# Kernel optimization log

Measured on AMD Instinct MI355X. Metric: run time of the kernel, lower is better.

## Reference

```python
import jax, jax.numpy as jnp
import numpy as np

B, R, A, S, SR = 128, 1024, 512, 196, 64


def _linear(x, w, b):
    return x @ w.T + b


def _lstm_cell(x, h, c, wih, whh, bih, bhh):
    # torch.nn.LSTMCell gate order: i, f, g, o
    g = x @ wih.T + bih + h @ whh.T + bhh
    i, f, gg, o = jnp.split(g, 4, axis=-1)
    c2 = jax.nn.sigmoid(f) * c + jax.nn.sigmoid(i) * jnp.tanh(gg)
    h2 = jax.nn.sigmoid(o) * jnp.tanh(c2)
    return h2, c2


def _attention(h, att_feats, p_att, mask, h2att_w, h2att_b, aw, ab):
    att_h = _linear(h, h2att_w, h2att_b)[:, None, :]            # [B,1,A]
    dot = jnp.tanh(p_att + att_h)                               # [B,S,A]
    e = jnp.einsum('bsa,a->bs', dot, aw[0]) + ab[0]             # alpha_net
    w = jax.nn.softmax(e, axis=1)
    w = w * mask
    w = w / jnp.sum(w, axis=1, keepdims=True)
    return jnp.einsum('bs,bsd->bd', w, att_feats)


def setup_inputs() -> dict:
    key = jax.random.key(0)
    ks = iter(jax.random.split(key, 80))
    def rn(shape, scale=1.0):
        return jax.random.normal(next(ks), shape, dtype=jnp.float32) * scale
    w = 0.02  # weight init scale
    inp = {
        'xt': rn((B, R)), 'state_h': rn((2, B, R)), 'state_c': rn((2, B, R)),
        'fc_feats': rn((B, R)),
        'att_feats': rn((B, S, R)), 'obj_feats': rn((B, S, R)),
        'attr_feats': rn((B, S, R)), 'rela_feats': rn((B, SR, R)),
        'p_obj_feats': rn((B, S, A)), 'p_attr_feats': rn((B, S, A)),
        'p_rela_feats': rn((B, SR, A)),
        'att_masks': jnp.ones((B, S), jnp.float32),
        'rela_masks': jnp.ones((B, SR), jnp.float32),
        'att_wih': rn((4*R, 3*R), w), 'att_whh': rn((4*R, R), w),
        'att_bih': rn((4*R,), w), 'att_bhh': rn((4*R,), w),
        'lang_wih': rn((4*R, 4*R), w), 'lang_whh': rn((4*R, R), w),
        'lang_bih': rn((4*R,), w), 'lang_bhh': rn((4*R,), w),
        'xt2_w': rn((R, R), w), 'xt2_b': rn((R,), w),
        'h_att2_w': rn((R, R), w), 'h_att2_b': rn((R,), w),
        'r_i2h_w': rn((R, 4*R), w), 'r_i2h_b': rn((R,), w),
        'r_h2h_w': rn((R, R), w), 'r_h2h_b': rn((R,), w),
        'huu_w': rn((R, 3*R), w), 'huu_b': rn((R,), w),
        'obj_h2att_w': rn((A, R), w), 'obj_h2att_b': rn((A,), w),
        'obj_alpha_w': rn((1, A), w), 'obj_alpha_b': rn((1,), w),
        'attr_h2att_w': rn((A, R), w), 'attr_h2att_b': rn((A,), w),
        'attr_alpha_w': rn((1, A), w), 'attr_alpha_b': rn((1,), w),
        'rela_h2att_w': rn((A, R), w), 'rela_h2att_b': rn((A,), w),
        'rela_alpha_w': rn((1, A), w), 'rela_alpha_b': rn((1,), w),
        'fr_lin_w': rn((R, R), w), 'fr_lin_b': rn((R,), w),
        'fr_emb_w': rn((R, R), w), 'fr_emb_b': rn((R,), w),
        'ho_lin_w': rn((R, R), w), 'ho_lin_b': rn((R,), w),
        'ho_emb_w': rn((R, R), w), 'ho_emb_b': rn((R,), w),
        'ada_alpha_w': rn((1, R), w), 'ada_alpha_b': rn((1,), w),
        'cfe_w': rn((R, A), w), 'cfe_b': rn((R,), w),
    }
    return inp


def reference(xt, state_h, state_c, fc_feats, att_feats, obj_feats, attr_feats,
              rela_feats, p_obj_feats, p_attr_feats, p_rela_feats, att_masks,
              rela_masks, att_wih, att_whh, att_bih, att_bhh, lang_wih,
              lang_whh, lang_bih, lang_bhh, xt2_w, xt2_b, h_att2_w, h_att2_b,
              r_i2h_w, r_i2h_b, r_h2h_w, r_h2h_b, huu_w, huu_b, obj_h2att_w,
              obj_h2att_b, obj_alpha_w, obj_alpha_b, attr_h2att_w,
              attr_h2att_b, attr_alpha_w, attr_alpha_b, rela_h2att_w,
              rela_h2att_b, rela_alpha_w, rela_alpha_b, fr_lin_w, fr_lin_b,
              fr_emb_w, fr_emb_b, ho_lin_w, ho_lin_b, ho_emb_w, ho_emb_b,
              ada_alpha_w, ada_alpha_b, cfe_w, cfe_b):
    # eval mode: all dropouts are identity
    prev_h = state_h[1]
    att_in = jnp.concatenate([prev_h, fc_feats, xt], axis=1)            # [B,3R]
    h_att_raw, c_att = _lstm_cell(att_in, state_h[0], state_c[0],
                                  att_wih, att_whh, att_bih, att_bhh)
    h_att = _linear(xt, xt2_w, xt2_b) + _linear(h_att_raw, h_att2_w, h_att2_b)
    att_obj = _attention(h_att, obj_feats, p_obj_feats, att_masks,
                         obj_h2att_w, obj_h2att_b, obj_alpha_w, obj_alpha_b)
    att_attr = _attention(h_att, attr_feats, p_attr_feats, att_masks,
                          attr_h2att_w, attr_h2att_b, attr_alpha_w, attr_alpha_b)
    att_rela = _attention(h_att, rela_feats, p_rela_feats, rela_masks,
                          rela_h2att_w, rela_h2att_b, rela_alpha_w, rela_alpha_b)
    lang_in = jnp.concatenate([h_att, att_obj, att_attr, att_rela], axis=1)  # [B,4R]
    h_lang, c_lang = _lstm_cell(lang_in, state_h[1], state_c[1],
                                lang_wih, lang_whh, lang_bih, lang_bhh)
    tanh_mt = jnp.tanh(c_lang)
    n5 = _linear(lang_in, r_i2h_w, r_i2h_b) + _linear(state_h[1], r_h2h_w, r_h2h_b)
    st = jax.nn.sigmoid(n5) * tanh_mt                                    # [B,R]
    # AdaAtt_attention(h_lang, st, att_feats, p_obj_feats)
    cfe = _linear(p_obj_feats, cfe_w, cfe_b)                             # [B,S,R]
    fake_region = jax.nn.relu(_linear(st, fr_lin_w, fr_lin_b))           # [B,R]
    fr_embed = _linear(fake_region, fr_emb_w, fr_emb_b)
    ho = jnp.tanh(_linear(h_lang, ho_lin_w, ho_lin_b))
    ho_embed = _linear(ho, ho_emb_w, ho_emb_b)
    img_all = jnp.concatenate([fake_region[:, None, :], att_feats], axis=1)    # [B,S+1,R]
    img_all_embed = jnp.concatenate([fr_embed[:, None, :], cfe], axis=1)
    hA = jnp.tanh(img_all_embed + ho_embed[:, None, :])
    e = jnp.einsum('bsr,r->bs', hA, ada_alpha_w[0]) + ada_alpha_b[0]
    PI = jax.nn.softmax(e, axis=1)                                       # [B,S+1]
    visAtt = jnp.einsum('bs,bsd->bd', PI, img_all)
    beta = PI[:, -1:]
    c_t_hat = beta * fake_region + (1.0 - beta) * visAtt
    output = _linear(jnp.concatenate([h_att, h_lang, c_t_hat], axis=1), huu_w, huu_b)
    new_h = jnp.stack([h_att, h_lang])
    new_c = jnp.stack([c_att, c_lang])
    return output, new_h, new_c
```

## Files before the change

kernel.cpp:

```cpp
#include <hip/hip_runtime.h>
#include <cstddef>

#define B 128
#define R 1024

typedef __attribute__((ext_vector_type(8))) short short8;
typedef __attribute__((ext_vector_type(4))) float f32x4;

__device__ __forceinline__ float sigf(float x) { return 1.0f / (1.0f + __expf(-x)); }

__device__ __forceinline__ short f2bf(float f) {
    unsigned int u = __float_as_uint(f);
    u += 0x7fff + ((u >> 16) & 1);
    return (short)(u >> 16);
}

__device__ __forceinline__ float bf2f(short s) {
    unsigned int u = ((unsigned int)(unsigned short)s) << 16;
    return __uint_as_float(u);
}

__device__ __forceinline__ short8 cvt8(float4 u, float4 v) {
    short8 r;
    r[0] = f2bf(u.x); r[1] = f2bf(u.y); r[2] = f2bf(u.z); r[3] = f2bf(u.w);
    r[4] = f2bf(v.x); r[5] = f2bf(v.y); r[6] = f2bf(v.z); r[7] = f2bf(v.w);
    return r;
}

__device__ __forceinline__ void gll16(const void* g, void* l) {
    __builtin_amdgcn_global_load_lds(
        (const __attribute__((address_space(1))) unsigned int*)g,
        (__attribute__((address_space(3))) unsigned int*)l, 16, 0, 0);
}

struct GJob {
    const float* A1; const float* A2; const float* A3;
    const float* W1; const float* W2; const float* W3;
    float* C;
    int lda1, lda2, lda3;
    int ldw1, ldw2, ldw3;
    int K1, K12, Ktot;
    int ldc, Kchunk, nb;
};

__global__ __launch_bounds__(256) void gemm_sk_kernel(GJob j0, GJob j1, GJob j2, int njobs)
{
    GJob j = j0;
    int nbx = blockIdx.x;
    if (njobs > 1 && nbx >= j.nb) { nbx -= j.nb; j = j1; }
    if (njobs > 2 && nbx >= j.nb) { nbx -= j.nb; j = j2; }

    const int bn   = nbx * 64;
    const int kbeg = blockIdx.y * j.Kchunk;
    const int kend = kbeg + j.Kchunk;

    __shared__ short sA[128 * 40];
    __shared__ short sB[64 * 40];
    const int tid  = threadIdx.x;
    const int rA   = tid >> 1;
    const int kha  = (tid & 1) << 4;
    const int rB   = tid >> 2;
    const int khb  = (tid & 3) << 3;
    const int lane = tid & 63;
    const int wid  = tid >> 6;
    const int wm   = wid * 32;
    const int fr_  = lane & 15;
    const int kof  = (lane >> 4) * 8;

    f32x4 acc[2][4];
#pragma unroll
    for (int m = 0; m < 2; ++m)
#pragma unroll
        for (int n = 0; n < 4; ++n)
            acc[m][n] = (f32x4)0.0f;

    for (int k0 = kbeg; k0 < kend; k0 += 32) {
        int kgA = k0 + kha;
        const float* pa;
        if (kgA < j.K1)       pa = j.A1 + (size_t)rA * j.lda1 + kgA;
        else if (kgA < j.K12) pa = j.A2 + (size_t)rA * j.lda2 + (kgA - j.K1);
        else                  pa = j.A3 + (size_t)rA * j.lda3 + (kgA - j.K12);
        int kgB = k0 + khb;
        const float* pw;
        if (kgB < j.K1)       pw = j.W1 + (size_t)(bn + rB) * j.ldw1 + kgB;
        else if (kgB < j.K12) pw = j.W2 + (size_t)(bn + rB) * j.ldw2 + (kgB - j.K1);
        else                  pw = j.W3 + (size_t)(bn + rB) * j.ldw3 + (kgB - j.K12);

        float4 a0 = ((const float4*)pa)[0];
        float4 a1 = ((const float4*)pa)[1];
        float4 a2 = ((const float4*)pa)[2];
        float4 a3 = ((const float4*)pa)[3];
        float4 w0 = ((const float4*)pw)[0];
        float4 w1 = ((const float4*)pw)[1];
        __syncthreads();
        *(short8*)&sA[rA * 40 + kha]     = cvt8(a0, a1);
        *(short8*)&sA[rA * 40 + kha + 8] = cvt8(a2, a3);
        *(short8*)&sB[rB * 40 + khb]     = cvt8(w0, w1);
        __syncthreads();
        short8 af[2], bf[4];
#pragma unroll
        for (int m = 0; m < 2; ++m)
            af[m] = *(const short8*)&sA[(wm + m * 16 + fr_) * 40 + kof];
#pragma unroll
        for (int n = 0; n < 4; ++n)
            bf[n] = *(const short8*)&sB[(n * 16 + fr_) * 40 + kof];
#pragma unroll
        for (int m = 0; m < 2; ++m)
#pragma unroll
            for (int n = 0; n < 4; ++n)
                acc[m][n] = __builtin_amdgcn_mfma_f32_16x16x32_bf16(af[m], bf[n], acc[m][n], 0, 0, 0);
    }

#pragma unroll
    for (int m = 0; m < 2; ++m) {
        int row0 = wm + m * 16 + ((lane >> 4) << 2);
#pragma unroll
        for (int n = 0; n < 4; ++n) {
            int col = bn + n * 16 + fr_;
#pragma unroll
            for (int rg = 0; rg < 4; ++rg)
                atomicAdd(&j.C[(size_t)(row0 + rg) * j.ldc + col], acc[m][n][rg]);
        }
    }
}

__global__ __launch_bounds__(256) void prologue_kernel(
    float* __restrict__ ws, int nws, float* __restrict__ o, const float* __restrict__ bias,
    const float* __restrict__ ph, const float* __restrict__ fc, const float* __restrict__ xt,
    float* __restrict__ att_in,
    const float* __restrict__ P, const float* __restrict__ W,
    short* __restrict__ Pbf, short* __restrict__ Wbf, int ZB)
{
    int blk = blockIdx.x;
    if (blk < ZB) {
        int idx = blk * 256 + threadIdx.x;
        if (idx < nws) ws[idx] = 0.0f;
        else if (idx < nws + 131072) { int i = idx - nws; o[i] = bias[i & 1023]; }
        return;
    }
    blk -= ZB;
    if (blk < 384) {
        int idx = blk * 256 + threadIdx.x;
        int r = idx / 768, c4 = idx - r * 768;
        int col = c4 * 4;
        const float* src = (col < 1024) ? (ph + (size_t)r * 1024 + col)
                         : (col < 2048) ? (fc + (size_t)r * 1024 + col - 1024)
                                        : (xt + (size_t)r * 1024 + col - 2048);
        *(float4*)(att_in + (size_t)r * 3072 + col) = *(const float4*)src;
        return;
    }
    blk -= 384;
    size_t base = ((size_t)blk * 256 + threadIdx.x) * 8;
    if (base < 12845056) {
        float4 u = *(const float4*)(P + base);
        float4 v = *(const float4*)(P + base + 4);
        *(short8*)(Pbf + base) = cvt8(u, v);
    } else {
        size_t i = base - 12845056;
        float4 u = *(const float4*)(W + i);
        float4 v = *(const float4*)(W + i + 4);
        *(short8*)(Wbf + i) = cvt8(u, v);
    }
}

template <bool PRE>
__global__ __launch_bounds__(256) void cfe_v3_kernel(
    const float* __restrict__ P, const short* __restrict__ Pbf,
    const float* __restrict__ Wf, const short* __restrict__ Wbf,
    const float* __restrict__ cb, const float* __restrict__ hoe,
    const float* __restrict__ ho_b, const float* __restrict__ aw,
    float* __restrict__ e)
{
    int p = blockIdx.x;
    int x8 = p & 7, rest = p >> 3;
    int n8 = rest & 7, q = rest >> 3;
    int m = q * 8 + x8;
    if (m >= 196) return;
    const int bm = m * 128, bn = n8 * 128;

    __shared__ short sA[128 * 64];
    __shared__ short sB[128 * 64];
    const int tid  = threadIdx.x;
    const int lane = tid & 63;
    const int wid  = tid >> 6;
    const int wm   = (wid >> 1) * 64;
    const int wn   = (wid & 1) * 64;
    const int fr_  = lane & 15;
    const int kof  = (lane >> 4) * 8;

    f32x4 acc[4][4];
#pragma unroll
    for (int mi = 0; mi < 4; ++mi)
#pragma unroll
        for (int n = 0; n < 4; ++n)
            acc[mi][n] = (f32x4)0.0f;

    for (int k0 = 0; k0 < 512; k0 += 64) {
        __syncthreads();
        if (PRE) {
#pragma unroll
            for (int i = 0; i < 4; ++i) {
                const short* ga = Pbf + (size_t)(bm + i * 32 + (tid >> 3)) * 512 + k0 + (tid & 7) * 8;
                gll16(ga, sA + wid * 512 + i * 2048);
                const short* gw = Wbf + (size_t)(bn + i * 32 + (tid >> 3)) * 512 + k0 + (tid & 7) * 8;
                gll16(gw, sB + wid * 512 + i * 2048);
            }
        } else {
            int row = tid >> 1;
            int half = (tid & 1) * 32;
            const float* pa = P + (size_t)(bm + row) * 512 + k0 + half;
            const float* pw = Wf + (size_t)(bn + row) * 512 + k0 + half;
#pragma unroll
            for (int c = 0; c < 32; c += 8) {
                float4 u = *(const float4*)(pa + c);
                float4 v = *(const float4*)(pa + c + 4);
                *(short8*)&sA[row * 64 + half + c] = cvt8(u, v);
                float4 uw = *(const float4*)(pw + c);
                float4 vw = *(const float4*)(pw + c + 4);
                *(short8*)&sB[row * 64 + half + c] = cvt8(uw, vw);
            }
        }
        __syncthreads();
#pragma unroll
        for (int ks = 0; ks < 64; ks += 32) {
            short8 af[4], bf[4];
#pragma unroll
            for (int mi = 0; mi < 4; ++mi)
                af[mi] = *(const short8*)&sA[(wm + mi * 16 + fr_) * 64 + ks + kof];
#pragma unroll
            for (int n = 0; n < 4; ++n)
                bf[n] = *(const short8*)&sB[(wn + n * 16 + fr_) * 64 + ks + kof];
#pragma unroll
            for (int mi = 0; mi < 4; ++mi)
#pragma unroll
                for (int n = 0; n < 4; ++n)
                    acc[mi][n] = __builtin_amdgcn_mfma_f32_16x16x32_bf16(af[mi], bf[n], acc[mi][n], 0, 0, 0);
        }
    }

    const int l4 = lane >> 4;
    const int rbase = bm + wm + (l4 << 2);
    const int b0 = rbase / 196;
    const int b1 = (rbase + 51) / 196;
    float cba[4], awa[4], hv0[4], hv1[4];
#pragma unroll
    for (int n = 0; n < 4; ++n) {
        int col = bn + wn + n * 16 + fr_;
        cba[n] = cb[col] + ho_b[col];
        awa[n] = aw[col];
        hv0[n] = hoe[(size_t)b0 * R + col];
        hv1[n] = hoe[(size_t)b1 * R + col];
    }
#pragma unroll
    for (int mi = 0; mi < 4; ++mi) {
#pragma unroll
        for (int rg = 0; rg < 4; ++rg) {
            int gr = rbase + mi * 16 + rg;
            int b = gr / 196;
            bool second = (b != b0);
            float part = 0.0f;
#pragma unroll
            for (int n = 0; n < 4; ++n) {
                float hv = second ? hv1[n] : hv0[n];
                part += tanhf(acc[mi][n][rg] + cba[n] + hv) * awa[n];
            }
            part += __shfl_xor(part, 1);
            part += __shfl_xor(part, 2);
            part += __shfl_xor(part, 4);
            part += __shfl_xor(part, 8);
            if (fr_ == 0)
                atomicAdd(&e[b * 197 + 1 + (gr - b * 196)], part);
        }
    }
}

__global__ __launch_bounds__(256) void lstm_kernel(
    float* __restrict__ g, const float* __restrict__ bih, const float* __restrict__ bhh,
    const float* __restrict__ cprev, float* __restrict__ h, float* __restrict__ c,
    const float* __restrict__ n5, const float* __restrict__ nb1,
    const float* __restrict__ nb2, float* __restrict__ st)
{
    int t = blockIdx.x * 256 + threadIdx.x;
    int b = t >> 8, d4 = (t & 255) * 4;
    float* gr = g + (size_t)b * 4096;
    float4 gi = *(float4*)(gr + d4);
    float4 gf = *(float4*)(gr + 1024 + d4);
    float4 gg = *(float4*)(gr + 2048 + d4);
    float4 go = *(float4*)(gr + 3072 + d4);
    float4 bi1 = *(const float4*)(bih + d4),        bh1 = *(const float4*)(bhh + d4);
    float4 bi2 = *(const float4*)(bih + 1024 + d4), bh2 = *(const float4*)(bhh + 1024 + d4);
    float4 bi3 = *(const float4*)(bih + 2048 + d4), bh3 = *(const float4*)(bhh + 2048 + d4);
    float4 bi4 = *(const float4*)(bih + 3072 + d4), bh4 = *(const float4*)(bhh + 3072 + d4);
    float4 cp = *(const float4*)(cprev + (size_t)b * 1024 + d4);
    float4 zero = {0.f, 0.f, 0.f, 0.f};
    *(float4*)(gr + d4) = zero; *(float4*)(gr + 1024 + d4) = zero;
    *(float4*)(gr + 2048 + d4) = zero; *(float4*)(gr + 3072 + d4) = zero;
    float4 cc, hh;
    float iv, fv, gv, ov, c2, tc;
    iv = sigf(gi.x + bi1.x + bh1.x); fv = sigf(gf.x + bi2.x + bh2.x);
    gv = tanhf(gg.x + bi3.x + bh3.x); ov = sigf(go.x + bi4.x + bh4.x);
    c2 = fv * cp.x + iv * gv; tc = tanhf(c2); cc.x = c2; hh.x = ov * tc;
    float tcx = tc;
    iv = sigf(gi.y + bi1.y + bh1.y); fv = sigf(gf.y + bi2.y + bh2.y);
    gv = tanhf(gg.y + bi3.y + bh3.y); ov = sigf(go.y + bi4.y + bh4.y);
    c2 = fv * cp.y + iv * gv; tc = tanhf(c2); cc.y = c2; hh.y = ov * tc;
    float tcy = tc;
    iv = sigf(gi.z + bi1.z + bh1.z); fv = sigf(gf.z + bi2.z + bh2.z);
    gv = tanhf(gg.z + bi3.z + bh3.z); ov = sigf(go.z + bi4.z + bh4.z);
    c2 = fv * cp.z + iv * gv; tc = tanhf(c2); cc.z = c2; hh.z = ov * tc;
    float tcz = tc;
    iv = sigf(gi.w + bi1.w + bh1.w); fv = sigf(gf.w + bi2.w + bh2.w);
    gv = tanhf(gg.w + bi3.w + bh3.w); ov = sigf(go.w + bi4.w + bh4.w);
    c2 = fv * cp.w + iv * gv; tc = tanhf(c2); cc.w = c2; hh.w = ov * tc;
    float tcw = tc;
    *(float4*)(c + (size_t)b * 1024 + d4) = cc;
    *(float4*)(h + (size_t)b * 1024 + d4) = hh;
    if (st) {
        float4 nv = *(const float4*)(n5 + (size_t)b * 1024 + d4);
        float4 n1 = *(const float4*)(nb1 + d4), n2 = *(const float4*)(nb2 + d4);
        float4 sv;
        sv.x = sigf(nv.x + n1.x + n2.x) * tcx;
        sv.y = sigf(nv.y + n1.y + n2.y) * tcy;
        sv.z = sigf(nv.z + n1.z + n2.z) * tcz;
        sv.w = sigf(nv.w + n1.w + n2.w) * tcw;
        *(float4*)(st + (size_t)b * 1024 + d4) = sv;
    }
}

__global__ __launch_bounds__(256) void hatt_epi_kernel(
    float* __restrict__ lang_in, const float* __restrict__ b1,
    const float* __restrict__ b2, float* __restrict__ h_att_out)
{
    int t = blockIdx.x * 256 + threadIdx.x;
    int r = t >> 8, c4 = (t & 255) * 4;
    float4 v = *(float4*)(lang_in + (size_t)r * 4096 + c4);
    float4 x1 = *(const float4*)(b1 + c4), x2 = *(const float4*)(b2 + c4);
    v.x += x1.x + x2.x; v.y += x1.y + x2.y; v.z += x1.z + x2.z; v.w += x1.w + x2.w;
    *(float4*)(lang_in + (size_t)r * 4096 + c4) = v;
    *(float4*)(h_att_out + (size_t)r * 1024 + c4) = v;
}

__global__ __launch_bounds__(256) void att_e3_kernel(
    const short* __restrict__ p0bf, const float* __restrict__ p1, const float* __restrict__ p2,
    const float* __restrict__ ah3,
    const float* __restrict__ b0, const float* __restrict__ b1, const float* __restrict__ b2,
    const float* __restrict__ aw0, const float* __restrict__ aw1, const float* __restrict__ aw2,
    float* __restrict__ e3)
{
    int wid = threadIdx.x >> 6, lane = threadIdx.x & 63;
    int idx = blockIdx.x * 4 + wid;
    float sum = 0.0f;
    if (idx < 25088) {
        int b = idx / 196;
        const short8 pv8 = *(const short8*)(p0bf + (size_t)idx * 512 + lane * 8);
        const float4* ab = (const float4*)(ah3 + (size_t)b * 512) + lane * 2;
        const float4* bb4 = (const float4*)b0 + lane * 2;
        const float4* aw4 = (const float4*)aw0 + lane * 2;
#pragma unroll
        for (int k = 0; k < 2; ++k) {
            float4 av = ab[k], bv = bb4[k], wv = aw4[k];
            sum += tanhf(bf2f(pv8[k * 4 + 0]) + av.x + bv.x) * wv.x;
            sum += tanhf(bf2f(pv8[k * 4 + 1]) + av.y + bv.y) * wv.y;
            sum += tanhf(bf2f(pv8[k * 4 + 2]) + av.z + bv.z) * wv.z;
            sum += tanhf(bf2f(pv8[k * 4 + 3]) + av.w + bv.w) * wv.w;
        }
    } else {
        const float* p; const float* bb; const float* aw; int S, loc, mod;
        if (idx < 50176) { mod = 1; loc = idx - 25088; p = p1; bb = b1; aw = aw1; S = 196; }
        else             { mod = 2; loc = idx - 50176; p = p2; bb = b2; aw = aw2; S = 64; }
        int b = loc / S;
        const float4* pr = (const float4*)(p + (size_t)loc * 512);
        const float4* ab = (const float4*)(ah3 + (size_t)mod * 65536 + (size_t)b * 512);
        const float4* bb4 = (const float4*)bb;
        const float4* aw4 = (const float4*)aw;
#pragma unroll
        for (int k = 0; k < 2; ++k) {
            int a = k * 64 + lane;
            float4 pv = pr[a], av = ab[a], bv = bb4[a], wv = aw4[a];
            sum += tanhf(pv.x + av.x + bv.x) * wv.x;
            sum += tanhf(pv.y + av.y + bv.y) * wv.y;
            sum += tanhf(pv.z + av.z + bv.z) * wv.z;
            sum += tanhf(pv.w + av.w + bv.w) * wv.w;
        }
    }
#pragma unroll
    for (int off = 32; off; off >>= 1) sum += __shfl_down(sum, off);
    if (lane == 0) e3[idx] = sum;
}

__global__ __launch_bounds__(256) void softmax3_kernel(
    float* __restrict__ e3, const float* __restrict__ am, const float* __restrict__ rm)
{
    __shared__ float red[256];
    int mod = blockIdx.x >> 7, b = blockIdx.x & 127, tid = threadIdx.x;
    int S = (mod == 2) ? 64 : 196;
    float* e = e3 + ((mod == 0) ? 0 : (mod == 1) ? 25088 : 50176) + (size_t)b * S;
    const float* mask = ((mod == 2) ? rm : am) + (size_t)b * S;
    float v = (tid < S) ? e[tid] : -3.4e38f;
    red[tid] = v; __syncthreads();
    for (int s = 128; s; s >>= 1) { if (tid < s) red[tid] = fmaxf(red[tid], red[tid + s]); __syncthreads(); }
    float m = red[0]; __syncthreads();
    float p = (tid < S) ? __expf(v - m) : 0.0f;
    red[tid] = p; __syncthreads();
    for (int s = 128; s; s >>= 1) { if (tid < s) red[tid] += red[tid + s]; __syncthreads(); }
    float s1 = red[0]; __syncthreads();
    float w = (tid < S) ? (p / s1) * mask[tid] : 0.0f;
    red[tid] = w; __syncthreads();
    for (int s = 128; s; s >>= 1) { if (tid < s) red[tid] += red[tid + s]; __syncthreads(); }
    float s2 = red[0];
    if (tid < S) e[tid] = w / s2;
}

__global__ __launch_bounds__(256) void wsum3_kernel(
    const float* __restrict__ e3,
    const float* __restrict__ f0, const float* __restrict__ f1, const float* __restrict__ f2,
    float* __restrict__ lang_in)
{
    int mod = blockIdx.x >> 7;
    int idx = (blockIdx.x & 127) * 256 + threadIdx.x;
    int b = idx >> 8, d4 = idx & 255;
    int S = (mod == 2) ? 64 : 196;
    int Sq = (S + 3) >> 2;
    int s0 = blockIdx.y * Sq, s1 = min(S, s0 + Sq);
    const float4* f = (const float4*)(((mod == 0) ? f0 : (mod == 1) ? f1 : f2) + ((size_t)b * S) * R) + d4;
    const float* wb = e3 + ((mod == 0) ? 0 : (mod == 1) ? 25088 : 50176) + (size_t)b * S;
    float4 acc = {0.f, 0.f, 0.f, 0.f};
#pragma unroll 4
    for (int s = s0; s < s1; ++s) {
        float w = wb[s];
        float4 fv = f[(size_t)s * 256];
        acc.x = fmaf(w, fv.x, acc.x); acc.y = fmaf(w, fv.y, acc.y);
        acc.z = fmaf(w, fv.z, acc.z); acc.w = fmaf(w, fv.w, acc.w);
    }
    float* dst = lang_in + (size_t)b * 4096 + 1024 + mod * 1024 + d4 * 4;
    atomicAdd(dst + 0, acc.x); atomicAdd(dst + 1, acc.y);
    atomicAdd(dst + 2, acc.z); atomicAdd(dst + 3, acc.w);
}

__global__ __launch_bounds__(256) void relutanh_kernel(
    float* __restrict__ fr, const float* __restrict__ frb,
    float* __restrict__ ho, const float* __restrict__ hob,
    float* __restrict__ ct_acc)
{
    int idx = blockIdx.x * 256 + threadIdx.x;
    int c = idx & 1023;
    if (idx < 131072) { fr[idx] = fmaxf(fr[idx] + frb[c], 0.0f); ct_acc[idx] = 0.0f; }
    else { int i = idx - 131072; ho[i] = tanhf(ho[i] + hob[c]); }
}

__global__ __launch_bounds__(256) void softmax_ada_kernel(
    float* __restrict__ e,
    const float* __restrict__ fre, const float* __restrict__ frb,
    const float* __restrict__ hoe, const float* __restrict__ hob,
    const float* __restrict__ aw)
{
    __shared__ float red[256];
    int b = blockIdx.x, tid = threadIdx.x;
    float s = 0.0f;
#pragma unroll
    for (int k = 0; k < 4; ++k) {
        int r = k * 256 + tid;
        s += tanhf(fre[(size_t)b * R + r] + frb[r] + hoe[(size_t)b * R + r] + hob[r]) * aw[r];
    }
    red[tid] = s; __syncthreads();
    for (int t = 128; t; t >>= 1) { if (tid < t) red[tid] += red[tid + t]; __syncthreads(); }
    float e0 = red[0]; __syncthreads();
    float v = (tid == 0) ? e0 : ((tid < 197) ? e[(size_t)b * 197 + tid] : -3.4e38f);
    red[tid] = v; __syncthreads();
    for (int t = 128; t; t >>= 1) { if (tid < t) red[tid] = fmaxf(red[tid], red[tid + t]); __syncthreads(); }
    float m = red[0]; __syncthreads();
    float p = (tid < 197) ? __expf(v - m) : 0.0f;
    red[tid] = p; __syncthreads();
    for (int t = 128; t; t >>= 1) { if (tid < t) red[tid] += red[tid + t]; __syncthreads(); }
    float s1 = red[0];
    if (tid < 197) e[(size_t)b * 197 + tid] = p / s1;
}

__global__ __launch_bounds__(256) void ct_part_kernel(
    const float* __restrict__ PI, const float* __restrict__ attf,
    float* __restrict__ ct_acc)
{
    int b = blockIdx.x, d4 = threadIdx.x;
    int s0 = blockIdx.y * 14, s1 = min(196, s0 + 14);
    const float* pb = PI + b * 197;
    const float4* af = (const float4*)(attf + ((size_t)b * 196) * R) + d4;
    float4 acc = {0.f, 0.f, 0.f, 0.f};
#pragma unroll 2
    for (int s = s0; s < s1; ++s) {
        float w = pb[1 + s];
        float4 av = af[(size_t)s * 256];
        acc.x = fmaf(w, av.x, acc.x); acc.y = fmaf(w, av.y, acc.y);
        acc.z = fmaf(w, av.z, acc.z); acc.w = fmaf(w, av.w, acc.w);
    }
    float* dst = ct_acc + (size_t)b * 1024 + d4 * 4;
    atomicAdd(dst + 0, acc.x); atomicAdd(dst + 1, acc.y);
    atomicAdd(dst + 2, acc.z); atomicAdd(dst + 3, acc.w);
}

__global__ __launch_bounds__(256) void ct_fin_kernel(
    const float* __restrict__ PI, const float* __restrict__ fr,
    const float* __restrict__ ct_acc, float* __restrict__ ct)
{
    int idx = blockIdx.x * 256 + threadIdx.x;
    int b = idx >> 10;
    const float* pb = PI + b * 197;
    float f = fr[idx];
    float acc = pb[0] * f + ct_acc[idx];
    float beta = pb[196];
    ct[idx] = beta * f + (1.0f - beta) * acc;
}

extern "C" void kernel_launch(void* const* d_in, const int* in_sizes, int n_in,
                              void* d_out, int out_size, void* d_ws, size_t ws_size,
                              hipStream_t stream)
{
    const float* xt         = (const float*)d_in[0];
    const float* state_h    = (const float*)d_in[1];
    const float* state_c    = (const float*)d_in[2];
    const float* fc_feats   = (const float*)d_in[3];
    const float* att_feats  = (const float*)d_in[4];
    const float* obj_feats  = (const float*)d_in[5];
    const float* attr_feats = (const float*)d_in[6];
    const float* rela_feats = (const float*)d_in[7];
    const float* p_obj      = (const float*)d_in[8];
    const float* p_attr     = (const float*)d_in[9];
    const float* p_rela     = (const float*)d_in[10];
    const float* att_masks  = (const float*)d_in[11];
    const float* rela_masks = (const float*)d_in[12];
    const float* att_wih    = (const float*)d_in[13];
    const float* att_whh    = (const float*)d_in[14];
    const float* att_bih    = (const float*)d_in[15];
    const float* att_bhh    = (const float*)d_in[16];
    const float* lang_wih   = (const float*)d_in[17];
    const float* lang_whh   = (const float*)d_in[18];
    const float* lang_bih   = (const float*)d_in[19];
    const float* lang_bhh   = (const float*)d_in[20];
    const float* xt2_w      = (const float*)d_in[21];
    const float* xt2_b      = (const float*)d_in[22];
    const float* h_att2_w   = (const float*)d_in[23];
    const float* h_att2_b   = (const float*)d_in[24];
    const float* r_i2h_w    = (const float*)d_in[25];
    const float* r_i2h_b    = (const float*)d_in[26];
    const float* r_h2h_w    = (const float*)d_in[27];
    const float* r_h2h_b    = (const float*)d_in[28];
    const float* huu_w      = (const float*)d_in[29];
    const float* huu_b      = (const float*)d_in[30];
    const float* obj_h2att_w  = (const float*)d_in[31];
    const float* obj_h2att_b  = (const float*)d_in[32];
    const float* obj_alpha_w  = (const float*)d_in[33];
    const float* attr_h2att_w = (const float*)d_in[35];
    const float* attr_h2att_b = (const float*)d_in[36];
    const float* attr_alpha_w = (const float*)d_in[37];
    const float* rela_h2att_w = (const float*)d_in[39];
    const float* rela_h2att_b = (const float*)d_in[40];
    const float* rela_alpha_w = (const float*)d_in[41];
    const float* fr_lin_w   = (const float*)d_in[43];
    const float* fr_lin_b   = (const float*)d_in[44];
    const float* fr_emb_w   = (const float*)d_in[45];
    const float* fr_emb_b   = (const float*)d_in[46];
    const float* ho_lin_w   = (const float*)d_in[47];
    const float* ho_lin_b   = (const float*)d_in[48];
    const float* ho_emb_w   = (const float*)d_in[49];
    const float* ho_emb_b   = (const float*)d_in[50];
    const float* ada_w      = (const float*)d_in[51];
    const float* cfe_w      = (const float*)d_in[53];
    const float* cfe_b      = (const float*)d_in[54];

    float* out = (float*)d_out;
    float* wsf = (float*)d_ws;

    float* g        = wsf + 0;
    float* lang_in  = wsf + 524288;
    float* att_h3   = wsf + 1048576;
    float* n5       = wsf + 1245184;
    float* fr       = wsf + 1376256;
    float* fre      = wsf + 1507328;
    float* ho       = wsf + 1638400;
    float* hoe      = wsf + 1769472;
    float* e_ada    = wsf + 1900544;
    const int NATOM = 1926144;
    float* att_in    = wsf + 1926144;
    float* ct_acc    = att_in;
    float* h_att_raw = wsf + 2319360;
    float* e3        = wsf + 2450432;
    float* st        = wsf + 2527232;
    float* ct        = wsf + 2658304;
    short* Pbf       = (short*)(wsf + 2789376);
    short* Wbf       = Pbf + 12845056;
    const bool big = ws_size >= (size_t)2789376 * 4 + (size_t)13369344 * 2;

    float* h_att_out  = out + 131072;
    float* h_lang_out = out + 262144;
    float* c_att_out  = out + 393216;
    float* c_lang_out = out + 524288;

    const float* prev_h = state_h + 131072;

    GJob Z = {};
    auto mk = [&](const float* A1, int lda1, int K1, const float* W1, int ldw1,
                  float* C, int ldc, int N, int Ktot, int Kchunk) {
        GJob j = Z;
        j.A1 = A1; j.lda1 = lda1; j.K1 = K1; j.K12 = Ktot; j.Ktot = Ktot;
        j.W1 = W1; j.ldw1 = ldw1;
        j.C = C; j.ldc = ldc; j.Kchunk = Kchunk; j.nb = N / 64;
        return j;
    };

    {
        const int ZB = (NATOM + 131072) / 256;
        int grid = ZB + 384 + (big ? 6528 : 0);
        prologue_kernel<<<grid, 256, 0, stream>>>(wsf, NATOM, out, huu_b,
            prev_h, fc_feats, xt, att_in, p_obj, cfe_w, Pbf, Wbf, ZB);
    }

    {
        GJob j = mk(att_in, 3072, 3072, att_wih, 3072, g, 4096, 4096, 4096, 512);
        j.A2 = state_h; j.lda2 = 1024; j.W2 = att_whh; j.ldw2 = 1024; j.K12 = 4096;
        gemm_sk_kernel<<<dim3(64, 8), 256, 0, stream>>>(j, Z, Z, 1);
    }
    lstm_kernel<<<128, 256, 0, stream>>>(g, att_bih, att_bhh, state_c, h_att_raw, c_att_out,
                                         nullptr, nullptr, nullptr, nullptr);

    {
        GJob j = mk(xt, 1024, 1024, xt2_w, 1024, lang_in, 4096, 1024, 2048, 128);
        j.A2 = h_att_raw; j.lda2 = 1024; j.W2 = h_att2_w; j.ldw2 = 1024; j.K12 = 2048;
        gemm_sk_kernel<<<dim3(16, 16), 256, 0, stream>>>(j, Z, Z, 1);
    }
    hatt_epi_kernel<<<128, 256, 0, stream>>>(lang_in, xt2_b, h_att2_b, h_att_out);

    {
        GJob j0 = mk(lang_in, 4096, 1024, obj_h2att_w,  1024, att_h3 + 0,      512, 512, 1024, 64);
        GJob j1 = mk(lang_in, 4096, 1024, attr_h2att_w, 1024, att_h3 + 65536,  512, 512, 1024, 64);
        GJob j2 = mk(lang_in, 4096, 1024, rela_h2att_w, 1024, att_h3 + 131072, 512, 512, 1024, 64);
        gemm_sk_kernel<<<dim3(24, 16), 256, 0, stream>>>(j0, j1, j2, 3);
    }
    att_e3_kernel<<<14592, 256, 0, stream>>>(Pbf, p_attr, p_rela, att_h3,
        obj_h2att_b, attr_h2att_b, rela_h2att_b, obj_alpha_w, attr_alpha_w, rela_alpha_w, e3);
    softmax3_kernel<<<384, 256, 0, stream>>>(e3, att_masks, rela_masks);
    wsum3_kernel<<<dim3(384, 4), 256, 0, stream>>>(e3, obj_feats, attr_feats, rela_feats, lang_in);

    {
        GJob j0 = mk(lang_in, 4096, 4096, lang_wih, 4096, g, 4096, 4096, 5120, 640);
        j0.A2 = prev_h; j0.lda2 = 1024; j0.W2 = lang_whh; j0.ldw2 = 1024; j0.K12 = 5120;
        GJob j1 = mk(lang_in, 4096, 4096, r_i2h_w, 4096, n5, 1024, 1024, 5120, 640);
        j1.A2 = prev_h; j1.lda2 = 1024; j1.W2 = r_h2h_w; j1.ldw2 = 1024; j1.K12 = 5120;
        gemm_sk_kernel<<<dim3(80, 8), 256, 0, stream>>>(j0, j1, Z, 2);
    }
    lstm_kernel<<<128, 256, 0, stream>>>(g, lang_bih, lang_bhh, state_c + 131072,
                                         h_lang_out, c_lang_out, n5, r_i2h_b, r_h2h_b, st);

    {
        GJob j0 = mk(st, 1024, 1024, fr_lin_w, 1024, fr, 1024, 1024, 1024, 64);
        GJob j1 = mk(h_lang_out, 1024, 1024, ho_lin_w, 1024, ho, 1024, 1024, 1024, 64);
        gemm_sk_kernel<<<dim3(32, 16), 256, 0, stream>>>(j0, j1, Z, 2);
    }
    relutanh_kernel<<<1024, 256, 0, stream>>>(fr, fr_lin_b, ho, ho_lin_b, ct_acc);

    {
        GJob j0 = mk(fr, 1024, 1024, fr_emb_w, 1024, fre, 1024, 1024, 1024, 64);
        GJob j1 = mk(ho, 1024, 1024, ho_emb_w, 1024, hoe, 1024, 1024, 1024, 64);
        gemm_sk_kernel<<<dim3(32, 16), 256, 0, stream>>>(j0, j1, Z, 2);
    }
    if (big) {
        cfe_v3_kernel<true><<<1600, 256, 0, stream>>>(p_obj, Pbf, cfe_w, Wbf,
            cfe_b, hoe, ho_emb_b, ada_w, e_ada);
    } else {
        cfe_v3_kernel<false><<<1600, 256, 0, stream>>>(p_obj, nullptr, cfe_w, nullptr,
            cfe_b, hoe, ho_emb_b, ada_w, e_ada);
    }
    softmax_ada_kernel<<<128, 256, 0, stream>>>(e_ada, fre, fr_emb_b, hoe, ho_emb_b, ada_w);
    ct_part_kernel<<<dim3(128, 14), 256, 0, stream>>>(e_ada, att_feats, ct_acc);
    ct_fin_kernel<<<512, 256, 0, stream>>>(e_ada, fr, ct_acc, ct);

    {
        GJob j = mk(lang_in, 4096, 1024, huu_w, 3072, out, 1024, 1024, 3072, 192);
        j.A2 = h_lang_out; j.lda2 = 1024; j.W2 = huu_w + 1024; j.ldw2 = 3072; j.K12 = 2048;
        j.A3 = ct; j.lda3 = 1024; j.W3 = huu_w + 2048; j.ldw3 = 3072;
        gemm_sk_kernel<<<dim3(16, 16), 256, 0, stream>>>(j, Z, Z, 1);
    }

    (void)in_sizes; (void)n_in; (void)out_size; (void)ws_size;
}
```

Baseline: 430.2 us.

## Pre-swizzle bf16 operands into MFMA fragment layout and load directly to registers

```diff
diff --git a/kernel.cpp b/kernel.cpp
--- a/kernel.cpp
+++ b/kernel.cpp
@@ -25,12 +25,6 @@
     r[0] = f2bf(u.x); r[1] = f2bf(u.y); r[2] = f2bf(u.z); r[3] = f2bf(u.w);
     r[4] = f2bf(v.x); r[5] = f2bf(v.y); r[6] = f2bf(v.z); r[7] = f2bf(v.w);
     return r;
-}
-
-__device__ __forceinline__ void gll16(const void* g, void* l) {
-    __builtin_amdgcn_global_load_lds(
-        (const __attribute__((address_space(1))) unsigned int*)g,
-        (__attribute__((address_space(3))) unsigned int*)l, 16, 0, 0);
 }
 
 struct GJob {
@@ -132,15 +126,16 @@
     short* __restrict__ Pbf, short* __restrict__ Wbf, int ZB)
 {
     int blk = blockIdx.x;
+    int tid = threadIdx.x;
     if (blk < ZB) {
-        int idx = blk * 256 + threadIdx.x;
+        int idx = blk * 256 + tid;
         if (idx < nws) ws[idx] = 0.0f;
         else if (idx < nws + 131072) { int i = idx - nws; o[i] = bias[i & 1023]; }
         return;
     }
     blk -= ZB;
     if (blk < 384) {
-        int idx = blk * 256 + threadIdx.x;
+        int idx = blk * 256 + tid;
         int r = idx / 768, c4 = idx - r * 768;
         int col = c4 * 4;
         const float* src = (col < 1024) ? (ph + (size_t)r * 1024 + col)
@@ -150,23 +145,27 @@
         return;
     }
     blk -= 384;
-    size_t base = ((size_t)blk * 256 + threadIdx.x) * 8;
-    if (base < 12845056) {
-        float4 u = *(const float4*)(P + base);
-        float4 v = *(const float4*)(P + base + 4);
-        *(short8*)(Pbf + base) = cvt8(u, v);
+    int lane = tid & 63;
+    int fr = lane & 15, kg = lane >> 4;
+    if (blk < 6272) {
+        int w = blk * 4 + (tid >> 6);
+        int rt = w >> 4, ks = w & 15;
+        const float* src = P + (size_t)(rt * 16 + fr) * 512 + ks * 32 + kg * 8;
+        float4 u = ((const float4*)src)[0];
+        float4 v = ((const float4*)src)[1];
+        *(short8*)(Pbf + ((size_t)w * 64 + lane) * 8) = cvt8(u, v);
     } else {
-        size_t i = base - 12845056;
-        float4 u = *(const float4*)(W + i);
-        float4 v = *(const float4*)(W + i + 4);
-        *(short8*)(Wbf + i) = cvt8(u, v);
-    }
-}
-
-template <bool PRE>
-__global__ __launch_bounds__(256) void cfe_v3_kernel(
-    const float* __restrict__ P, const short* __restrict__ Pbf,
-    const float* __restrict__ Wf, const short* __restrict__ Wbf,
+        int w = (blk - 6272) * 4 + (tid >> 6);
+        int ct = w >> 4, ks = w & 15;
+        const float* src = W + (size_t)(ct * 16 + fr) * 512 + ks * 32 + kg * 8;
+        float4 u = ((const float4*)src)[0];
+        float4 v = ((const float4*)src)[1];
+        *(short8*)(Wbf + ((size_t)w * 64 + lane) * 8) = cvt8(u, v);
+    }
+}
+
+__global__ __launch_bounds__(256) void cfe_v4_kernel(
+    const short* __restrict__ Pbf, const short* __restrict__ Wbf,
     const float* __restrict__ cb, const float* __restrict__ hoe,
     const float* __restrict__ ho_b, const float* __restrict__ aw,
     float* __restrict__ e)
@@ -178,8 +177,93 @@
     if (m >= 196) return;
     const int bm = m * 128, bn = n8 * 128;
 
-    __shared__ short sA[128 * 64];
-    __shared__ short sB[128 * 64];
+    const int tid  = threadIdx.x;
+    const int lane = tid & 63;
+    const int wid  = tid >> 6;
+    const int wm   = (wid >> 1) * 64;
+    const int wn   = (wid & 1) * 64;
+    const int fr_  = lane & 15;
+
+    const int rtb = (bm + wm) >> 4;
+    const int ctb = (bn + wn) >> 4;
+
+    const short* pA = Pbf + ((size_t)rtb * 16) * 512 + lane * 8;
+    const short* pB = Wbf + ((size_t)ctb * 16) * 512 + lane * 8;
+
+    f32x4 acc[4][4];
+#pragma unroll
+    for (int mi = 0; mi < 4; ++mi)
+#pragma unroll
+        for (int n = 0; n < 4; ++n)
+            acc[mi][n] = (f32x4)0.0f;
+
+#pragma unroll 2
+    for (int ks = 0; ks < 16; ++ks) {
+        short8 af[4], bf[4];
+#pragma unroll
+        for (int mi = 0; mi < 4; ++mi)
+            af[mi] = *(const short8*)(pA + ((size_t)mi * 16 + ks) * 512);
+#pragma unroll
+        for (int n = 0; n < 4; ++n)
+            bf[n] = *(const short8*)(pB + ((size_t)n * 16 + ks) * 512);
+#pragma unroll
+        for (int mi = 0; mi < 4; ++mi)
+#pragma unroll
+            for (int n = 0; n < 4; ++n)
+                acc[mi][n] = __builtin_amdgcn_mfma_f32_16x16x32_bf16(af[mi], bf[n], acc[mi][n], 0, 0, 0);
+    }
+
+    const int l4 = lane >> 4;
+    const int rbase = bm + wm + (l4 << 2);
+    const int b0 = rbase / 196;
+    const int b1 = (rbase + 51) / 196;
+    float cba[4], awa[4], hv0[4], hv1[4];
+#pragma unroll
+    for (int n = 0; n < 4; ++n) {
+        int col = bn + wn + n * 16 + fr_;
+        cba[n] = cb[col] + ho_b[col];
+        awa[n] = aw[col];
+        hv0[n] = hoe[(size_t)b0 * R + col];
+        hv1[n] = hoe[(size_t)b1 * R + col];
+    }
+#pragma unroll
+    for (int mi = 0; mi < 4; ++mi) {
+#pragma unroll
+        for (int rg = 0; rg < 4; ++rg) {
+            int gr = rbase + mi * 16 + rg;
+            int b = gr / 196;
+            bool second = (b != b0);
+            float part = 0.0f;
+#pragma unroll
+            for (int n = 0; n < 4; ++n) {
+                float hv = second ? hv1[n] : hv0[n];
+                part += tanhf(acc[mi][n][rg] + cba[n] + hv) * awa[n];
+            }
+            part += __shfl_xor(part, 1);
+            part += __shfl_xor(part, 2);
+            part += __shfl_xor(part, 4);
+            part += __shfl_xor(part, 8);
+            if (fr_ == 0)
+                atomicAdd(&e[b * 197 + 1 + (gr - b * 196)], part);
+        }
+    }
+}
+
+__global__ __launch_bounds__(256) void cfe_fallback_kernel(
+    const float* __restrict__ P, const float* __restrict__ Wf,
+    const float* __restrict__ cb, const float* __restrict__ hoe,
+    const float* __restrict__ ho_b, const float* __restrict__ aw,
+    float* __restrict__ e)
+{
+    int p = blockIdx.x;
+    int x8 = p & 7, rest = p >> 3;
+    int n8 = rest & 7, q = rest >> 3;
+    int m = q * 8 + x8;
+    if (m >= 196) return;
+    const int bm = m * 128, bn = n8 * 128;
+
+    __shared__ short sA[128 * 72];
+    __shared__ short sB[128 * 72];
     const int tid  = threadIdx.x;
     const int lane = tid & 63;
     const int wid  = tid >> 6;
@@ -197,28 +281,18 @@
 
     for (int k0 = 0; k0 < 512; k0 += 64) {
         __syncthreads();
-        if (PRE) {
-#pragma unroll
-            for (int i = 0; i < 4; ++i) {
-                const short* ga = Pbf + (size_t)(bm + i * 32 + (tid >> 3)) * 512 + k0 + (tid & 7) * 8;
-                gll16(ga, sA + wid * 512 + i * 2048);
-                const short* gw = Wbf + (size_t)(bn + i * 32 + (tid >> 3)) * 512 + k0 + (tid & 7) * 8;
-                gll16(gw, sB + wid * 512 + i * 2048);
-            }
-        } else {
-            int row = tid >> 1;
-            int half = (tid & 1) * 32;
-            const float* pa = P + (size_t)(bm + row) * 512 + k0 + half;
-            const float* pw = Wf + (size_t)(bn + row) * 512 + k0 + half;
-#pragma unroll
-            for (int c = 0; c < 32; c += 8) {
-                float4 u = *(const float4*)(pa + c);
-                float4 v = *(const float4*)(pa + c + 4);
-                *(short8*)&sA[row * 64 + half + c] = cvt8(u, v);
-                float4 uw = *(const float4*)(pw + c);
-                float4 vw = *(const float4*)(pw + c + 4);
-                *(short8*)&sB[row * 64 + half + c] = cvt8(uw, vw);
-            }
+        int row = tid >> 1;
+        int half = (tid & 1) * 32;
+        const float* pa = P + (size_t)(bm + row) * 512 + k0 + half;
+        const float* pw = Wf + (size_t)(bn + row) * 512 + k0 + half;
+#pragma unroll
+        for (int c = 0; c < 32; c += 8) {
+            float4 u = *(const float4*)(pa + c);
+            float4 v = *(const float4*)(pa + c + 4);
+            *(short8*)&sA[row * 72 + half + c] = cvt8(u, v);
+            float4 uw = *(const float4*)(pw + c);
+            float4 vw = *(const float4*)(pw + c + 4);
+            *(short8*)&sB[row * 72 + half + c] = cvt8(uw, vw);
         }
         __syncthreads();
 #pragma unroll
@@ -226,10 +300,10 @@
             short8 af[4], bf[4];
 #pragma unroll
             for (int mi = 0; mi < 4; ++mi)
-                af[mi] = *(const short8*)&sA[(wm + mi * 16 + fr_) * 64 + ks + kof];
+                af[mi] = *(const short8*)&sA[(wm + mi * 16 + fr_) * 72 + ks + kof];
 #pragma unroll
             for (int n = 0; n < 4; ++n)
-                bf[n] = *(const short8*)&sB[(wn + n * 16 + fr_) * 64 + ks + kof];
+                bf[n] = *(const short8*)&sB[(wn + n * 16 + fr_) * 72 + ks + kof];
 #pragma unroll
             for (int mi = 0; mi < 4; ++mi)
 #pragma unroll
@@ -340,8 +414,10 @@
     *(float4*)(h_att_out + (size_t)r * 1024 + c4) = v;
 }
 
+template <bool PRE>
 __global__ __launch_bounds__(256) void att_e3_kernel(
-    const short* __restrict__ p0bf, const float* __restrict__ p1, const float* __restrict__ p2,
+    const short* __restrict__ p0bf, const float* __restrict__ p0f,
+    const float* __restrict__ p1, const float* __restrict__ p2,
     const float* __restrict__ ah3,
     const float* __restrict__ b0, const float* __restrict__ b1, const float* __restrict__ b2,
     const float* __restrict__ aw0, const float* __restrict__ aw1, const float* __restrict__ aw2,
@@ -352,17 +428,31 @@
     float sum = 0.0f;
     if (idx < 25088) {
         int b = idx / 196;
-        const short8 pv8 = *(const short8*)(p0bf + (size_t)idx * 512 + lane * 8);
         const float4* ab = (const float4*)(ah3 + (size_t)b * 512) + lane * 2;
         const float4* bb4 = (const float4*)b0 + lane * 2;
         const float4* aw4 = (const float4*)aw0 + lane * 2;
-#pragma unroll
-        for (int k = 0; k < 2; ++k) {
-            float4 av = ab[k], bv = bb4[k], wv = aw4[k];
-            sum += tanhf(bf2f(pv8[k * 4 + 0]) + av.x + bv.x) * wv.x;
-            sum += tanhf(bf2f(pv8[k * 4 + 1]) + av.y + bv.y) * wv.y;
-            sum += tanhf(bf2f(pv8[k * 4 + 2]) + av.z + bv.z) * wv.z;
-            sum += tanhf(bf2f(pv8[k * 4 + 3]) + av.w + bv.w) * wv.w;
+        if (PRE) {
+            int rt = idx >> 4, fr = idx & 15;
+            const short8 pv8 = *(const short8*)(p0bf +
+                (((size_t)(rt * 16 + (lane >> 2)) * 64 + (lane & 3) * 16 + fr) * 8));
+#pragma unroll
+            for (int k = 0; k < 2; ++k) {
+                float4 av = ab[k], bv = bb4[k], wv = aw4[k];
+                sum += tanhf(bf2f(pv8[k * 4 + 0]) + av.x + bv.x) * wv.x;
+                sum += tanhf(bf2f(pv8[k * 4 + 1]) + av.y + bv.y) * wv.y;
+                sum += tanhf(bf2f(pv8[k * 4 + 2]) + av.z + bv.z) * wv.z;
+                sum += tanhf(bf2f(pv8[k * 4 + 3]) + av.w + bv.w) * wv.w;
+            }
+        } else {
+            const float4* pr = (const float4*)(p0f + (size_t)idx * 512) + lane * 2;
+#pragma unroll
+            for (int k = 0; k < 2; ++k) {
+                float4 pv = pr[k], av = ab[k], bv = bb4[k], wv = aw4[k];
+                sum += tanhf(pv.x + av.x + bv.x) * wv.x;
+                sum += tanhf(pv.y + av.y + bv.y) * wv.y;
+                sum += tanhf(pv.z + av.z + bv.z) * wv.z;
+                sum += tanhf(pv.w + av.w + bv.w) * wv.w;
+            }
         }
     } else {
         const float* p; const float* bb; const float* aw; int S, loc, mod;
@@ -634,8 +724,12 @@
         GJob j2 = mk(lang_in, 4096, 1024, rela_h2att_w, 1024, att_h3 + 131072, 512, 512, 1024, 64);
         gemm_sk_kernel<<<dim3(24, 16), 256, 0, stream>>>(j0, j1, j2, 3);
     }
-    att_e3_kernel<<<14592, 256, 0, stream>>>(Pbf, p_attr, p_rela, att_h3,
-        obj_h2att_b, attr_h2att_b, rela_h2att_b, obj_alpha_w, attr_alpha_w, rela_alpha_w, e3);
+    if (big)
+        att_e3_kernel<true><<<14592, 256, 0, stream>>>(Pbf, p_obj, p_attr, p_rela, att_h3,
+            obj_h2att_b, attr_h2att_b, rela_h2att_b, obj_alpha_w, attr_alpha_w, rela_alpha_w, e3);
+    else
+        att_e3_kernel<false><<<14592, 256, 0, stream>>>(nullptr, p_obj, p_attr, p_rela, att_h3,
+            obj_h2att_b, attr_h2att_b, rela_h2att_b, obj_alpha_w, attr_alpha_w, rela_alpha_w, e3);
     softmax3_kernel<<<384, 256, 0, stream>>>(e3, att_masks, rela_masks);
     wsum3_kernel<<<dim3(384, 4), 256, 0, stream>>>(e3, obj_feats, attr_feats, rela_feats, lang_in);
 
@@ -662,11 +756,9 @@
         gemm_sk_kernel<<<dim3(32, 16), 256, 0, stream>>>(j0, j1, Z, 2);
     }
     if (big) {
-        cfe_v3_kernel<true><<<1600, 256, 0, stream>>>(p_obj, Pbf, cfe_w, Wbf,
-            cfe_b, hoe, ho_emb_b, ada_w, e_ada);
+        cfe_v4_kernel<<<1600, 256, 0, stream>>>(Pbf, Wbf, cfe_b, hoe, ho_emb_b, ada_w, e_ada);
     } else {
-        cfe_v3_kernel<false><<<1600, 256, 0, stream>>>(p_obj, nullptr, cfe_w, nullptr,
-            cfe_b, hoe, ho_emb_b, ada_w, e_ada);
+        cfe_fallback_kernel<<<1600, 256, 0, stream>>>(p_obj, cfe_w, cfe_b, hoe, ho_emb_b, ada_w, e_ada);
     }
     softmax_ada_kernel<<<128, 256, 0, stream>>>(e_ada, fre, fr_emb_b, hoe, ho_emb_b, ada_w);
     ct_part_kernel<<<dim3(128, 14), 256, 0, stream>>>(e_ada, att_feats, ct_acc);
```

Measured after the change: 437.0 us. About the same (+1.6%).
